# Kernel tuning notes

Hardware: AMD Instinct MI355X
Metric: run time of the kernel (lower is better)

The kernel has to match this reference:

```python
import jax, jax.numpy as jnp
import numpy as np

DIM = 512
N_TOK = 256
BATCH = 512
HIDDEN = int(DIM * 0.2)          # 102
KEEPED = int(256 * 0.5 * 0.4)    # 51 aggregated tokens
NUM_KEEP = int(np.ceil(N_TOK * 0.5))  # 128 kept tokens
EPS_NORM = 1e-12
EPS_LN = 1e-5


def _l2norm(v, axis=-1):
    n = jnp.linalg.norm(v, axis=axis, keepdims=True)
    return v / jnp.maximum(n, EPS_NORM)


def setup_inputs() -> dict:
    key = jax.random.key(0)
    ks = jax.random.split(key, 8)
    x = jax.random.normal(ks[0], (BATCH, N_TOK, DIM), dtype=jnp.float32)
    cross_attention = jax.random.normal(ks[1], (BATCH, N_TOK), dtype=jnp.float32)
    # TokenAggregation params: LayerNorm(dim) -> Linear(dim,hidden) -> GELU -> Linear(hidden,keeped)
    ln_g = jnp.ones((DIM,), jnp.float32)
    ln_b = jnp.zeros((DIM,), jnp.float32)
    s1 = 1.0 / np.sqrt(DIM)
    W1 = jax.random.uniform(ks[2], (DIM, HIDDEN), jnp.float32, -s1, s1)
    b1 = jax.random.uniform(ks[3], (HIDDEN,), jnp.float32, -s1, s1)
    s2 = 1.0 / np.sqrt(HIDDEN)
    W2 = jax.random.uniform(ks[4], (HIDDEN, KEEPED), jnp.float32, -s2, s2)
    b2 = jax.random.uniform(ks[5], (KEEPED,), jnp.float32, -s2, s2)
    scale = jnp.ones((1, 1, 1), jnp.float32)
    return {"x": x, "cross_attention": cross_attention, "ln_g": ln_g, "ln_b": ln_b,
            "W1": W1, "b1": b1, "W2": W2, "b2": b2, "scale": scale}


def reference(x, cross_attention, ln_g, ln_b, W1, b1, W2, b2, scale):
    # ---- scoring: cosine similarity of each token with the mean token ----
    glo = _l2norm(jnp.mean(x, axis=1, keepdims=True))          # [B,1,C]
    self_att = jnp.sum(glo * _l2norm(x), axis=-1)              # [B,N]
    score = self_att + cross_attention                         # [B,N]

    # ---- TokenSparse: sort descending, split keep / non-keep ----
    idx = jnp.argsort(-score, axis=1)                          # [B,N]
    score_sort = jnp.take_along_axis(score, idx, axis=1)       # [B,N] descending
    keep_idx = idx[:, :NUM_KEEP]                               # [B,K]
    non_idx = idx[:, NUM_KEEP:]                                # [B,N-K]
    sel = jnp.take_along_axis(x, keep_idx[:, :, None], axis=1)       # [B,K,C]
    non = jnp.take_along_axis(x, non_idx[:, :, None], axis=1)        # [B,N-K,C]
    non_w = jax.nn.softmax(score_sort[:, NUM_KEEP:], axis=1)[:, :, None]
    extra = jnp.sum(non * non_w, axis=1, keepdims=True)        # [B,1,C]

    # ---- TokenAggregation: LN -> MLP -> softmax weights -> bmm ----
    mu = jnp.mean(sel, axis=-1, keepdims=True)
    var = jnp.mean((sel - mu) ** 2, axis=-1, keepdims=True)
    h = (sel - mu) / jnp.sqrt(var + EPS_LN) * ln_g + ln_b
    h = jax.nn.gelu(h @ W1 + b1, approximate=False)            # [B,K,H]
    w = h @ W2 + b2                                            # [B,K,P]
    w = jnp.swapaxes(w, 1, 2) * scale                          # [B,P,K]
    w = jax.nn.softmax(w, axis=2)
    aggr = jnp.einsum('bpk,bkc->bpc', w, sel)                  # [B,P,C]

    return jnp.concatenate([aggr, extra], axis=1)              # [B,P+1,C]
```

## Files before the change

kernel.cpp:

```cpp
#include <hip/hip_runtime.h>

#define BB 512
#define TT 256
#define DD 512
#define HH 102
#define PP 51
#define NKEEP 128

typedef unsigned short u16;
typedef unsigned int u32;
typedef unsigned long long u64;
typedef float f32x4 __attribute__((ext_vector_type(4)));
typedef short s16x8 __attribute__((ext_vector_type(8)));

#define MFMA16(A, B, C) __builtin_amdgcn_mfma_f32_16x16x32_bf16((A), (B), (C), 0, 0, 0)

#define GLOAD16(gsrc, ldst)                                                     \
  __builtin_amdgcn_global_load_lds(                                             \
      (const __attribute__((address_space(1))) u32*)(gsrc),                     \
      (__attribute__((address_space(3))) u32*)(ldst), 16, 0, 0)

static __device__ __forceinline__ float bf2f(u16 u) {
  u32 v = ((u32)u) << 16;
  float f;
  __builtin_memcpy(&f, &v, 4);
  return f;
}
static __device__ __forceinline__ u16 f2bf(float f) {
  u32 v;
  __builtin_memcpy(&v, &f, 4);
  u32 r = v + 0x7fffu + ((v >> 16) & 1u);
  return (u16)(r >> 16);
}
static __device__ __forceinline__ u32 cvtpk(float a, float b) {
  u32 r;
  asm("v_cvt_pk_bf16_f32 %0, %1, %2" : "=v"(r) : "v"(a), "v"(b));
  return r;
}
static __device__ __forceinline__ float flo16(u32 u) {
  u32 v = u << 16;
  float f;
  __builtin_memcpy(&f, &v, 4);
  return f;
}
static __device__ __forceinline__ float fhi16(u32 u) {
  u32 v = u & 0xffff0000u;
  float f;
  __builtin_memcpy(&f, &v, 4);
  return f;
}
static __device__ __forceinline__ s16x8 mkfrag4(u32 a, u32 b, u32 c, u32 d) {
  u32 t[4] = {a, b, c, d};
  s16x8 f;
  __builtin_memcpy(&f, t, 16);
  return f;
}
static __device__ __forceinline__ s16x8 mkfrag2(u64 a, u64 b) {
  u64 t[2] = {a, b};
  s16x8 f;
  __builtin_memcpy(&f, t, 16);
  return f;
}
static __device__ __forceinline__ u64 trread(u32 addr, int imm) {
  u64 d;
  asm volatile("ds_read_b64_tr_b16 %0, %1 offset:%2" : "=v"(d) : "v"(addr), "i"(imm));
  return d;
}

__global__ __launch_bounds__(1024, 8) void k_score(
    const float* __restrict__ x, const float* __restrict__ ca,
    const float* __restrict__ w1, const float* __restrict__ w2,
    float* __restrict__ out, int* __restrict__ keepg,
    float* __restrict__ muk, float* __restrict__ ivk,
    u16* __restrict__ w1th, u16* __restrict__ w1tl,
    u16* __restrict__ w2th, u16* __restrict__ w2tl) {
  const int tid = threadIdx.x;

  if (blockIdx.x >= BB) {
    const int e0 = (blockIdx.x - BB) * 4096;
#pragma unroll
    for (int i = 0; i < 4; ++i) {
      const int e = e0 + i * 1024 + tid;
      if (e < 57344) {
        const int p = e >> 9, k = e & 511;
        const float v = (p < HH) ? w1[(size_t)k * HH + p] : 0.f;
        const u16 hi = f2bf(v);
        w1th[e] = hi;
        w1tl[e] = f2bf(v - bf2f(hi));
      } else {
        const int e2 = e - 57344;
        const int p = e2 >> 7, j = e2 & 127;
        const float v = (p < PP && j < HH) ? w2[(size_t)j * PP + p] : 0.f;
        const u16 hi = f2bf(v);
        w2th[e2] = hi;
        w2tl[e2] = f2bf(v - bf2f(hi));
      }
    }
    return;
  }

  __shared__ float part[8 * 512];
  __shared__ float glo[DD];
  __shared__ float sc[TT];
  __shared__ float ss[TT];
  __shared__ int perm[TT];
  __shared__ float wq[NKEEP];
  __shared__ float red[128];
  __shared__ float mls[TT], ils[TT];
  int* pc = (int*)part;

  const int b = blockIdx.x;
  const float* xb = x + (size_t)b * TT * DD;

  {
    int c4 = (tid & 127) * 4, tg = tid >> 7;
    float4 a = {0.f, 0.f, 0.f, 0.f};
    const float* p0 = xb + tg * 32 * DD + c4;
    for (int t = 0; t < 32; ++t) {
      float4 v = *(const float4*)(p0 + t * DD);
      a.x += v.x; a.y += v.y; a.z += v.z; a.w += v.w;
    }
    *(float4*)&part[tg * 512 + c4] = a;
  }
  __syncthreads();
  if (tid < 128) {
    int c4 = tid * 4;
    float4 m = {0.f, 0.f, 0.f, 0.f};
    for (int g = 0; g < 8; ++g) {
      float4 v = *(const float4*)&part[g * 512 + c4];
      m.x += v.x; m.y += v.y; m.z += v.z; m.w += v.w;
    }
    m.x *= (1.f / TT); m.y *= (1.f / TT); m.z *= (1.f / TT); m.w *= (1.f / TT);
    *(float4*)&glo[c4] = m;
    red[tid] = m.x * m.x + m.y * m.y + m.z * m.z + m.w * m.w;
  }
  __syncthreads();
  for (int s = 64; s > 0; s >>= 1) {
    if (tid < s) red[tid] += red[tid + s];
    __syncthreads();
  }
  if (tid < 128) {
    float inv = 1.f / fmaxf(sqrtf(red[0]), 1e-12f);
    int c4 = tid * 4;
    float4 m = *(float4*)&glo[c4];
    m.x *= inv; m.y *= inv; m.z *= inv; m.w *= inv;
    *(float4*)&glo[c4] = m;
  }
  __syncthreads();

  {
    const int w = tid >> 6, lane = tid & 63;
    float gl[8];
#pragma unroll
    for (int j = 0; j < 8; ++j) gl[j] = glo[lane * 8 + j];
    for (int i = 0; i < 16; ++i) {
      int t = w * 16 + i;
      const float* xr = xb + t * DD + lane * 8;
      float4 r0 = *(const float4*)xr;
      float4 r1 = *(const float4*)(xr + 4);
      float vs[8] = {r0.x, r0.y, r0.z, r0.w, r1.x, r1.y, r1.z, r1.w};
      float s1 = 0.f, s2 = 0.f, dt = 0.f;
#pragma unroll
      for (int j = 0; j < 8; ++j) {
        s1 += vs[j];
        s2 += vs[j] * vs[j];
        dt += vs[j] * gl[j];
      }
      for (int m = 32; m; m >>= 1) {
        s1 += __shfl_xor(s1, m);
        s2 += __shfl_xor(s2, m);
        dt += __shfl_xor(dt, m);
      }
      if (lane == 0) {
        sc[t] = dt / fmaxf(sqrtf(s2), 1e-12f) + ca[b * TT + t];
        float mu = s1 * (1.f / DD);
        float var = s2 * (1.f / DD) - mu * mu;
        mls[t] = mu;
        ils[t] = rsqrtf(var + 1e-5f);
      }
    }
  }
  __syncthreads();

  {
    int t = tid & 255, ch = tid >> 8;
    float st = sc[t];
    int cnt = 0;
    for (int j = ch * 64; j < ch * 64 + 64; ++j) {
      float sj = sc[j];
      cnt += (sj > st) || (sj == st && j < t);
    }
    pc[ch * 256 + t] = cnt;
  }
  __syncthreads();
  if (tid < 256) {
    int rank = pc[tid] + pc[256 + tid] + pc[512 + tid] + pc[768 + tid];
    perm[rank] = tid;
    ss[rank] = sc[tid];
  }
  __syncthreads();

  if (tid < 128) {
    float e = expf(ss[NKEEP + tid] - ss[NKEEP]);
    wq[tid] = e;
    red[tid] = e;
  }
  __syncthreads();
  for (int s = 64; s > 0; s >>= 1) {
    if (tid < s) red[tid] += red[tid + s];
    __syncthreads();
  }
  if (tid < 128) {
    wq[tid] *= (1.f / red[0]);
    const int pm = perm[tid];
    keepg[b * NKEEP + tid] = pm;
    muk[b * NKEEP + tid] = mls[pm];
    ivk[b * NKEEP + tid] = ils[pm];
  }
  __syncthreads();

  {
    int c4 = (tid & 127) * 4, tg = tid >> 7;
    float4 a = {0.f, 0.f, 0.f, 0.f};
    for (int q = tg * 16; q < tg * 16 + 16; ++q) {
      int tok = perm[NKEEP + q] & 255;
      float w = wq[q];
      float4 v = *(const float4*)(xb + tok * DD + c4);
      a.x += w * v.x; a.y += w * v.y; a.z += w * v.z; a.w += w * v.w;
    }
    *(float4*)&part[tg * 512 + c4] = a;
  }
  __syncthreads();
  if (tid < 128) {
    int c4 = tid * 4;
    float4 m = {0.f, 0.f, 0.f, 0.f};
    for (int g = 0; g < 8; ++g) {
      float4 v = *(const float4*)&part[g * 512 + c4];
      m.x += v.x; m.y += v.y; m.z += v.z; m.w += v.w;
    }
    *(float4*)(out + ((size_t)b * 52 + 51) * DD + c4) = m;
  }
}

__global__ __launch_bounds__(512, 2) void k_fused(
    const float* __restrict__ x,
    const u16* __restrict__ w1th, const u16* __restrict__ w1tl,
    const u16* __restrict__ w2th, const u16* __restrict__ w2tl,
    const float* __restrict__ lng, const float* __restrict__ lnb,
    const float* __restrict__ b1, const float* __restrict__ b2,
    const float* __restrict__ scale, const int* __restrict__ keepg,
    const float* __restrict__ mukg, const float* __restrict__ ivkg,
    float* __restrict__ out) {
  __shared__ __align__(16) char pool[66560];
  __shared__ __align__(16) float lnGs[DD], lnBs[DD];
  __shared__ float mus[NKEEP], ivs[NKEEP];
  __shared__ int keeps[NKEEP];
  __shared__ float b1s[112], b2s[64];
  __shared__ float sscale;

  const int b = blockIdx.x;
  const int tid = threadIdx.x;
  const int w = tid >> 6;
  const int lane = tid & 63;
  const int cl = lane & 15;
  const int g2 = lane >> 4;

  if (tid < NKEEP) {
    keeps[tid] = keepg[b * NKEEP + tid] & 255;
    mus[tid] = mukg[b * NKEEP + tid];
    ivs[tid] = ivkg[b * NKEEP + tid];
  }
  for (int i = tid; i < DD; i += 512) {
    lnGs[i] = lng[i];
    lnBs[i] = lnb[i];
  }
  if (tid < 112) b1s[tid] = (tid < HH) ? b1[tid] : 0.f;
  if (tid < 64) b2s[tid] = (tid < PP) ? b2[tid] : 0.f;
  if (tid == 0) sscale = scale[0];
  __syncthreads();

  const float* xb = x + (size_t)b * TT * DD;

  const int rowm = 16 * w + cl;
  const int tok = keeps[rowm];
  const float mu = mus[rowm], iv = ivs[rowm];
  const float nmuiv = -mu * iv;
  const float* xrow = xb + (size_t)tok * DD;

  const int swz7 = cl & 7;
  const int bA0 = cl * 128 + ((g2 ^ swz7) << 4);
  const int bA1 = cl * 128 + (((4 + g2) ^ swz7) << 4);

  f32x4 acc1[7];
#pragma unroll
  for (int n = 0; n < 7; ++n) acc1[n] = (f32x4){0.f, 0.f, 0.f, 0.f};

#define STAGE_W1(tt, dst)                                                      \
  {                                                                            \
    _Pragma("unroll") for (int i_ = 0; i_ < 4; ++i_) {                         \
      const int j_ = w + 8 * i_;                                               \
      if (j_ < 28) {                                                           \
        const int s_ = j_ * 64 + lane;                                         \
        const int part_ = (j_ >= 14);                                          \
        const int sr_ = s_ - part_ * 896;                                      \
        const int row_ = sr_ >> 3, uu_ = sr_ & 7;                              \
        const u16* src_ = (part_ ? w1tl : w1th) + row_ * 512 + (tt)*64 +       \
                          ((uu_ ^ (row_ & 7)) << 3);                           \
        GLOAD16(src_, (dst) + j_ * 1024);                                      \
      }                                                                        \
    }                                                                          \
  }

  float4 xc0 = *(const float4*)(xrow + g2 * 8);
  float4 xc1 = *(const float4*)(xrow + g2 * 8 + 4);
  float4 xc2 = *(const float4*)(xrow + 32 + g2 * 8);
  float4 xc3 = *(const float4*)(xrow + 32 + g2 * 8 + 4);
  STAGE_W1(0, pool);
  __syncthreads();

#pragma unroll 1
  for (int t = 0; t < 8; ++t) {
    float4 xn0, xn1, xn2, xn3;
    if (t < 7) {
      STAGE_W1(t + 1, pool + ((t + 1) & 1) * 28672);
      const float* xr2 = xrow + (t + 1) * 64 + g2 * 8;
      xn0 = *(const float4*)xr2;
      xn1 = *(const float4*)(xr2 + 4);
      xn2 = *(const float4*)(xr2 + 32);
      xn3 = *(const float4*)(xr2 + 36);
    }
    const char* wbr = pool + (t & 1) * 28672;
#pragma unroll
    for (int kh = 0; kh < 2; ++kh) {
      const int d0 = t * 64 + kh * 32 + g2 * 8;
      const float4 xv0 = kh ? xc2 : xc0;
      const float4 xv1 = kh ? xc3 : xc1;
      const float4 gg0 = *(const float4*)&lnGs[d0];
      const float4 gg1 = *(const float4*)&lnGs[d0 + 4];
      const float4 bb0 = *(const float4*)&lnBs[d0];
      const float4 bb1 = *(const float4*)&lnBs[d0 + 4];
      float y0 = fmaf(fmaf(xv0.x, iv, nmuiv), gg0.x, bb0.x);
      float y1 = fmaf(fmaf(xv0.y, iv, nmuiv), gg0.y, bb0.y);
      float y2 = fmaf(fmaf(xv0.z, iv, nmuiv), gg0.z, bb0.z);
      float y3 = fmaf(fmaf(xv0.w, iv, nmuiv), gg0.w, bb0.w);
      float y4 = fmaf(fmaf(xv1.x, iv, nmuiv), gg1.x, bb1.x);
      float y5 = fmaf(fmaf(xv1.y, iv, nmuiv), gg1.y, bb1.y);
      float y6 = fmaf(fmaf(xv1.z, iv, nmuiv), gg1.z, bb1.z);
      float y7 = fmaf(fmaf(xv1.w, iv, nmuiv), gg1.w, bb1.w);
      u32 h01 = cvtpk(y0, y1), h23 = cvtpk(y2, y3);
      u32 h45 = cvtpk(y4, y5), h67 = cvtpk(y6, y7);
      u32 l01 = cvtpk(y0 - flo16(h01), y1 - fhi16(h01));
      u32 l23 = cvtpk(y2 - flo16(h23), y3 - fhi16(h23));
      u32 l45 = cvtpk(y4 - flo16(h45), y5 - fhi16(h45));
      u32 l67 = cvtpk(y6 - flo16(h67), y7 - fhi16(h67));
      const s16x8 fh = mkfrag4(h01, h23, h45, h67);
      const s16x8 fl = mkfrag4(l01, l23, l45, l67);
      const int bA = kh ? bA1 : bA0;
#pragma unroll
      for (int n = 0; n < 7; ++n) {
        const s16x8 bh = *(const s16x8*)(wbr + n * 2048 + bA);
        const s16x8 bl = *(const s16x8*)(wbr + 14336 + n * 2048 + bA);
        acc1[n] = MFMA16(fh, bh, acc1[n]);
        acc1[n] = MFMA16(fl, bh, acc1[n]);
        acc1[n] = MFMA16(fh, bl, acc1[n]);
      }
    }
    __syncthreads();
    if (t < 7) { xc0 = xn0; xc1 = xn1; xc2 = xn2; xc3 = xn3; }
  }

  char* W2b = pool + 32768;
  {
#pragma unroll
    for (int i = 0; i < 4; ++i) {
      const int j2 = w + 8 * i;
      const int part = (j2 >= 16);
      const int jj = j2 - part * 16;
      const int s = jj * 64 + lane;
      const int row = s >> 4, uu = s & 15;
      const u16* src = (part ? w2tl : w2th) + row * 128 + ((uu ^ (row & 15)) << 3);
      GLOAD16(src, W2b + part * 16384 + jj * 1024);
    }
  }
#pragma unroll
  for (int n = 0; n < 7; ++n) {
    const int col = 16 * n + cl;
    const float bia = b1s[col];
#pragma unroll
    for (int r = 0; r < 4; ++r) {
      const int row = 16 * w + 4 * g2 + r;
      float v = acc1[n][r] + bia;
      float ge = 0.5f * v * (1.f + erff(v * 0.70710678118f));
      const int byteoff = (row * 256 + col * 2) ^ ((row & 7) << 4);
      *(u16*)(pool + byteoff) = f2bf(ge);
    }
  }
  for (int i = tid; i < 1024; i += 512) {
    const int row = i >> 3;
    const int col = 112 + 2 * (i & 7);
    const int byteoff = (row * 256 + col * 2) ^ ((row & 7) << 4);
    *(u32*)(pool + byteoff) = 0u;
  }
  __syncthreads();

  f32x4 acc2[4];
#pragma unroll
  for (int n = 0; n < 4; ++n) acc2[n] = (f32x4){0.f, 0.f, 0.f, 0.f};
  {
    const int row2 = 16 * w + cl;
#pragma unroll
    for (int kk = 0; kk < 4; ++kk) {
      const int byteoff = (row2 * 256 + kk * 64 + g2 * 16) ^ ((row2 & 7) << 4);
      const s16x8 ha = *(const s16x8*)(pool + byteoff);
      const int bB = cl * 256 + (((kk * 4 + g2) ^ cl) << 4);
#pragma unroll
      for (int n = 0; n < 4; ++n) {
        const s16x8 bh = *(const s16x8*)(W2b + n * 4096 + bB);
        const s16x8 bl = *(const s16x8*)(W2b + 16384 + n * 4096 + bB);
        acc2[n] = MFMA16(ha, bh, acc2[n]);
        acc2[n] = MFMA16(ha, bl, acc2[n]);
      }
    }
  }
  __syncthreads();
  float* wt = (float*)(pool + 32768);
  {
    const float scv = sscale;
#pragma unroll
    for (int n = 0; n < 4; ++n) {
      const int p = 16 * n + cl;
#pragma unroll
      for (int r = 0; r < 4; ++r) {
        const int k = 16 * w + 4 * g2 + r;
        wt[p * 132 + k] = (acc2[n][r] + b2s[p]) * scv;
      }
    }
  }
  __syncthreads();

  for (int p = w; p < PP; p += 8) {
    float v0 = wt[p * 132 + lane], v1 = wt[p * 132 + 64 + lane];
    float mx = fmaxf(v0, v1);
    for (int m = 32; m; m >>= 1) mx = fmaxf(mx, __shfl_xor(mx, m));
    float e0 = expf(v0 - mx), e1 = expf(v1 - mx);
    float s = e0 + e1;
    for (int m = 32; m; m >>= 1) s += __shfl_xor(s, m);
    float is = 1.f / s;
    wt[p * 132 + lane] = e0 * is;
    wt[p * 132 + 64 + lane] = e1 * is;
  }
  __syncthreads();

  const int mb = w >> 2;
  const int nsub = w & 3;

  const int c4g = tid & 15;
  const int k0 = tid >> 4;
  const float* xcb = xb + 4 * c4g;
  const int tk0 = keeps[k0], tk1 = keeps[k0 + 32];
  const int tk2 = keeps[k0 + 64], tk3 = keeps[k0 + 96];
  const int base_b = (((c4g >> 2) * 2 + ((k0 >> 2) & 1)) << 9) +
                     ((k0 >> 3) << 7) + ((k0 & 3) << 5) + ((c4g & 3) << 3);

  float4 pv0 = *(const float4*)(xcb + (size_t)tk0 * DD);
  float4 pv1 = *(const float4*)(xcb + (size_t)tk1 * DD);
  float4 pv2 = *(const float4*)(xcb + (size_t)tk2 * DD);
  float4 pv3 = *(const float4*)(xcb + (size_t)tk3 * DD);

  s16x8 ah0[4], al0[4], ah1[4], al1[4];
  {
    const int pr0 = 32 * mb + cl;
    const int pr1 = pr0 + 16;
#pragma unroll
    for (int kk = 0; kk < 4; ++kk) {
      f32x4 wa = *(const f32x4*)&wt[pr0 * 132 + kk * 32 + 8 * g2];
      f32x4 wb = *(const f32x4*)&wt[pr0 * 132 + kk * 32 + 8 * g2 + 4];
      u32 a0 = cvtpk(wa.x, wa.y), a1 = cvtpk(wa.z, wa.w);
      u32 a2 = cvtpk(wb.x, wb.y), a3 = cvtpk(wb.z, wb.w);
      ah0[kk] = mkfrag4(a0, a1, a2, a3);
      al0[kk] = mkfrag4(cvtpk(wa.x - flo16(a0), wa.y - fhi16(a0)),
                        cvtpk(wa.z - flo16(a1), wa.w - fhi16(a1)),
                        cvtpk(wb.x - flo16(a2), wb.y - fhi16(a2)),
                        cvtpk(wb.z - flo16(a3), wb.w - fhi16(a3)));
      f32x4 wc = *(const f32x4*)&wt[pr1 * 132 + kk * 32 + 8 * g2];
      f32x4 wd = *(const f32x4*)&wt[pr1 * 132 + kk * 32 + 8 * g2 + 4];
      u32 c0 = cvtpk(wc.x, wc.y), c1 = cvtpk(wc.z, wc.w);
      u32 c2 = cvtpk(wd.x, wd.y), c3 = cvtpk(wd.z, wd.w);
      ah1[kk] = mkfrag4(c0, c1, c2, c3);
      al1[kk] = mkfrag4(cvtpk(wc.x - flo16(c0), wc.y - fhi16(c0)),
                        cvtpk(wc.z - flo16(c1), wc.w - fhi16(c1)),
                        cvtpk(wd.x - flo16(c2), wd.y - fhi16(c2)),
                        cvtpk(wd.z - flo16(c3), wd.w - fhi16(c3)));
    }
  }
  const u32 trbase = (u32)(size_t)pool + nsub * 1024 + g2 * 128 + 8 * cl;

#define SELW(v, bo)                                                            \
  {                                                                            \
    u32 h01_ = cvtpk((v).x, (v).y), h23_ = cvtpk((v).z, (v).w);                \
    u32 q01_ = cvtpk((v).x - flo16(h01_), (v).y - fhi16(h01_));                \
    u32 q23_ = cvtpk((v).z - flo16(h23_), (v).w - fhi16(h23_));                \
    *(u64*)(pool + (bo)) = ((u64)h23_ << 32) | h01_;                           \
    *(u64*)(pool + 16384 + (bo)) = ((u64)q23_ << 32) | q01_;                   \
  }

#pragma unroll 1
  for (int ch = 0; ch < 8; ++ch) {
    SELW(pv0, base_b);
    SELW(pv1, base_b + 4096);
    SELW(pv2, base_b + 8192);
    SELW(pv3, base_b + 12288);
    __syncthreads();
    float4 nv0, nv1, nv2, nv3;
    if (ch < 7) {
      const float* xnp = xcb + (ch + 1) * 64;
      nv0 = *(const float4*)(xnp + (size_t)tk0 * DD);
      nv1 = *(const float4*)(xnp + (size_t)tk1 * DD);
      nv2 = *(const float4*)(xnp + (size_t)tk2 * DD);
      nv3 = *(const float4*)(xnp + (size_t)tk3 * DD);
    }
    f32x4 acg0 = (f32x4){0.f, 0.f, 0.f, 0.f};
    f32x4 acg1 = (f32x4){0.f, 0.f, 0.f, 0.f};
    u64 th[4][2], tl[4][2];
#pragma unroll
    for (int kk = 0; kk < 4; ++kk) {
      th[kk][0] = trread(trbase, kk * 4096);
      th[kk][1] = trread(trbase, kk * 4096 + 512);
      tl[kk][0] = trread(trbase, kk * 4096 + 16384);
      tl[kk][1] = trread(trbase, kk * 4096 + 16896);
    }
    asm volatile("s_waitcnt lgkmcnt(0)" ::: "memory");
    __builtin_amdgcn_sched_barrier(0);
#pragma unroll
    for (int kk = 0; kk < 4; ++kk) {
      const s16x8 bh = mkfrag2(th[kk][0], th[kk][1]);
      const s16x8 bl = mkfrag2(tl[kk][0], tl[kk][1]);
      acg0 = MFMA16(ah0[kk], bh, acg0);
      acg0 = MFMA16(al0[kk], bh, acg0);
      acg0 = MFMA16(ah0[kk], bl, acg0);
      acg1 = MFMA16(ah1[kk], bh, acg1);
      acg1 = MFMA16(al1[kk], bh, acg1);
      acg1 = MFMA16(ah1[kk], bl, acg1);
    }
    const int ccol = ch * 64 + 16 * nsub + cl;
#pragma unroll
    for (int r = 0; r < 4; ++r) {
      const int p0 = 32 * mb + 4 * g2 + r;
      if (p0 < PP) out[((size_t)b * 52 + p0) * DD + ccol] = acg0[r];
      const int p1 = 32 * mb + 16 + 4 * g2 + r;
      if (p1 < PP) out[((size_t)b * 52 + p1) * DD + ccol] = acg1[r];
    }
    __syncthreads();
    if (ch < 7) { pv0 = nv0; pv1 = nv1; pv2 = nv2; pv3 = nv3; }
  }
}

extern "C" void kernel_launch(void* const* d_in, const int* in_sizes, int n_in,
                              void* d_out, int out_size, void* d_ws, size_t ws_size,
                              hipStream_t stream) {
  const float* x = (const float*)d_in[0];
  const float* ca = (const float*)d_in[1];
  const float* lng = (const float*)d_in[2];
  const float* lnb = (const float*)d_in[3];
  const float* w1 = (const float*)d_in[4];
  const float* b1 = (const float*)d_in[5];
  const float* w2 = (const float*)d_in[6];
  const float* b2 = (const float*)d_in[7];
  const float* scale = (const float*)d_in[8];
  float* out = (float*)d_out;

  char* ws = (char*)d_ws;
  int* keepg = (int*)ws;
  float* muk = (float*)(ws + 262144);
  float* ivk = (float*)(ws + 524288);
  u16* w1th = (u16*)(ws + 786432);
  u16* w1tl = (u16*)(ws + 901120);
  u16* w2th = (u16*)(ws + 1015808);
  u16* w2tl = (u16*)(ws + 1032192);

  k_score<<<BB + 16, 1024, 0, stream>>>(x, ca, w1, w2, out, keepg, muk, ivk,
                                        w1th, w1tl, w2th, w2tl);
  k_fused<<<BB, 512, 0, stream>>>(x, w1th, w1tl, w2th, w2tl, lng, lnb, b1, b2,
                                  scale, keepg, muk, ivk, out);
}
```

Measured before the change: 523.2 us.

## Fuse column-sum and per-token stats into a single pass over x

The scoring kernel used to read each batch's x tile twice: once for the token mean and again for the per-token norm, mean/var and dot with the global mean. It now walks x once in 64-column chunks. Each thread keeps its 16 values in registers while the chunk column sums are reduced through a swizzled LDS buffer, and the dot product is accumulated against those unnormalised sums, with normalisation applied at the end. This halves global reads in this phase at the cost of three barriers per chunk and a larger LDS footprint that may lower occupancy.

```diff
diff --git a/kernel.cpp b/kernel.cpp
--- a/kernel.cpp
+++ b/kernel.cpp
@@ -99,98 +99,119 @@
     return;
   }
 
-  __shared__ float part[8 * 512];
-  __shared__ float glo[DD];
+  __shared__ __align__(16) float xls[256 * 64];
+  __shared__ float part2[1024];
+  __shared__ float cs[64];
+  __shared__ float ctot[512];
   __shared__ float sc[TT];
   __shared__ float ss[TT];
   __shared__ int perm[TT];
   __shared__ float wq[NKEEP];
   __shared__ float red[128];
-  __shared__ float mls[TT], ils[TT];
-  int* pc = (int*)part;
+
+  int* pc = (int*)xls;
+  float* part5 = xls;
+  float* mls = part2;
+  float* ils = part2 + 256;
 
   const int b = blockIdx.x;
   const float* xb = x + (size_t)b * TT * DD;
 
+  const int r = tid >> 2;
+  const int q = tid & 3;
+  const int r7 = r & 7;
+  const int rgA = tid >> 6, jA = tid & 63;
+  const int uA = jA >> 2, sA = jA & 3;
+
+  float s1p = 0.f, s2p = 0.f, dtp = 0.f;
+
+#pragma unroll 1
+  for (int ch = 0; ch < 8; ++ch) {
+    const float* xp = xb + (size_t)r * DD + ch * 64 + q * 16;
+    const float4 v0 = *(const float4*)xp;
+    const float4 v1 = *(const float4*)(xp + 4);
+    const float4 v2 = *(const float4*)(xp + 8);
+    const float4 v3 = *(const float4*)(xp + 12);
+    s1p += (v0.x + v0.y + v0.z + v0.w) + (v1.x + v1.y + v1.z + v1.w) +
+           (v2.x + v2.y + v2.z + v2.w) + (v3.x + v3.y + v3.z + v3.w);
+    s2p += v0.x * v0.x + v0.y * v0.y + v0.z * v0.z + v0.w * v0.w +
+           v1.x * v1.x + v1.y * v1.y + v1.z * v1.z + v1.w * v1.w +
+           v2.x * v2.x + v2.y * v2.y + v2.z * v2.z + v2.w * v2.w +
+           v3.x * v3.x + v3.y * v3.y + v3.z * v3.z + v3.w * v3.w;
+    *(float4*)&xls[r * 64 + (((q * 4 + 0) ^ r7) << 2)] = v0;
+    *(float4*)&xls[r * 64 + (((q * 4 + 1) ^ r7) << 2)] = v1;
+    *(float4*)&xls[r * 64 + (((q * 4 + 2) ^ r7) << 2)] = v2;
+    *(float4*)&xls[r * 64 + (((q * 4 + 3) ^ r7) << 2)] = v3;
+    __syncthreads();
+    {
+      float a = 0.f;
+#pragma unroll
+      for (int rr = 0; rr < 16; ++rr) {
+        a += xls[(rgA * 16 + rr) * 64 + ((uA ^ (rr & 7)) << 2) + sA];
+      }
+      part2[rgA * 64 + jA] = a;
+    }
+    __syncthreads();
+    if (tid < 64) {
+      float c = 0.f;
+#pragma unroll
+      for (int g = 0; g < 16; ++g) c += part2[g * 64 + tid];
+      cs[tid] = c;
+      ctot[ch * 64 + tid] = c;
+    }
+    __syncthreads();
+    {
+      const float4 c0 = *(const float4*)&cs[q * 16];
+      const float4 c1 = *(const float4*)&cs[q * 16 + 4];
+      const float4 c2 = *(const float4*)&cs[q * 16 + 8];
+      const float4 c3 = *(const float4*)&cs[q * 16 + 12];
+      dtp += v0.x * c0.x + v0.y * c0.y + v0.z * c0.z + v0.w * c0.w +
+             v1.x * c1.x + v1.y * c1.y + v1.z * c1.z + v1.w * c1.w +
+             v2.x * c2.x + v2.y * c2.y + v2.z * c2.z + v2.w * c2.w +
+             v3.x * c3.x + v3.y * c3.y + v3.z * c3.z + v3.w * c3.w;
+    }
+  }
+  __syncthreads();
+
+  if (tid < 512) {
+    float cv = ctot[tid];
+    float v = cv * cv;
+    for (int m = 32; m; m >>= 1) v += __shfl_xor(v, m);
+    if ((tid & 63) == 0) red[tid >> 6] = v;
+  }
+  __syncthreads();
+  if (tid == 0) {
+    float cn2 = red[0] + red[1] + red[2] + red[3] + red[4] + red[5] + red[6] + red[7];
+    cs[0] = 1.f / fmaxf(sqrtf(cn2) * (1.f / 256.f), 1e-12f);
+  }
+  __syncthreads();
+
   {
-    int c4 = (tid & 127) * 4, tg = tid >> 7;
-    float4 a = {0.f, 0.f, 0.f, 0.f};
-    const float* p0 = xb + tg * 32 * DD + c4;
-    for (int t = 0; t < 32; ++t) {
-      float4 v = *(const float4*)(p0 + t * DD);
-      a.x += v.x; a.y += v.y; a.z += v.z; a.w += v.w;
-    }
-    *(float4*)&part[tg * 512 + c4] = a;
-  }
-  __syncthreads();
-  if (tid < 128) {
-    int c4 = tid * 4;
-    float4 m = {0.f, 0.f, 0.f, 0.f};
-    for (int g = 0; g < 8; ++g) {
-      float4 v = *(const float4*)&part[g * 512 + c4];
-      m.x += v.x; m.y += v.y; m.z += v.z; m.w += v.w;
-    }
-    m.x *= (1.f / TT); m.y *= (1.f / TT); m.z *= (1.f / TT); m.w *= (1.f / TT);
-    *(float4*)&glo[c4] = m;
-    red[tid] = m.x * m.x + m.y * m.y + m.z * m.z + m.w * m.w;
-  }
-  __syncthreads();
-  for (int s = 64; s > 0; s >>= 1) {
-    if (tid < s) red[tid] += red[tid + s];
-    __syncthreads();
-  }
-  if (tid < 128) {
-    float inv = 1.f / fmaxf(sqrtf(red[0]), 1e-12f);
-    int c4 = tid * 4;
-    float4 m = *(float4*)&glo[c4];
-    m.x *= inv; m.y *= inv; m.z *= inv; m.w *= inv;
-    *(float4*)&glo[c4] = m;
+    float a1 = s1p, a2 = s2p, ad = dtp;
+    a1 += __shfl_xor(a1, 1); a1 += __shfl_xor(a1, 2);
+    a2 += __shfl_xor(a2, 1); a2 += __shfl_xor(a2, 2);
+    ad += __shfl_xor(ad, 1); ad += __shfl_xor(ad, 2);
+    if (q == 0) {
+      const float invc = cs[0];
+      const float self = ad * (1.f / 256.f) * invc;
+      sc[r] = self / fmaxf(sqrtf(a2), 1e-12f) + ca[b * TT + r];
+      const float mu = a1 * (1.f / DD);
+      const float var = a2 * (1.f / DD) - mu * mu;
+      mls[r] = mu;
+      ils[r] = rsqrtf(var + 1e-5f);
+    }
   }
   __syncthreads();
 
   {
-    const int w = tid >> 6, lane = tid & 63;
-    float gl[8];
-#pragma unroll
-    for (int j = 0; j < 8; ++j) gl[j] = glo[lane * 8 + j];
-    for (int i = 0; i < 16; ++i) {
-      int t = w * 16 + i;
-      const float* xr = xb + t * DD + lane * 8;
-      float4 r0 = *(const float4*)xr;
-      float4 r1 = *(const float4*)(xr + 4);
-      float vs[8] = {r0.x, r0.y, r0.z, r0.w, r1.x, r1.y, r1.z, r1.w};
-      float s1 = 0.f, s2 = 0.f, dt = 0.f;
-#pragma unroll
-      for (int j = 0; j < 8; ++j) {
-        s1 += vs[j];
-        s2 += vs[j] * vs[j];
-        dt += vs[j] * gl[j];
-      }
-      for (int m = 32; m; m >>= 1) {
-        s1 += __shfl_xor(s1, m);
-        s2 += __shfl_xor(s2, m);
-        dt += __shfl_xor(dt, m);
-      }
-      if (lane == 0) {
-        sc[t] = dt / fmaxf(sqrtf(s2), 1e-12f) + ca[b * TT + t];
-        float mu = s1 * (1.f / DD);
-        float var = s2 * (1.f / DD) - mu * mu;
-        mls[t] = mu;
-        ils[t] = rsqrtf(var + 1e-5f);
-      }
-    }
-  }
-  __syncthreads();
-
-  {
-    int t = tid & 255, ch = tid >> 8;
+    int t = tid & 255, chh = tid >> 8;
     float st = sc[t];
     int cnt = 0;
-    for (int j = ch * 64; j < ch * 64 + 64; ++j) {
+    for (int j = chh * 64; j < chh * 64 + 64; ++j) {
       float sj = sc[j];
       cnt += (sj > st) || (sj == st && j < t);
     }
-    pc[ch * 256 + t] = cnt;
+    pc[chh * 256 + t] = cnt;
   }
   __syncthreads();
   if (tid < 256) {
@@ -222,20 +243,20 @@
   {
     int c4 = (tid & 127) * 4, tg = tid >> 7;
     float4 a = {0.f, 0.f, 0.f, 0.f};
-    for (int q = tg * 16; q < tg * 16 + 16; ++q) {
-      int tok = perm[NKEEP + q] & 255;
-      float w = wq[q];
+    for (int qq = tg * 16; qq < tg * 16 + 16; ++qq) {
+      int tok = perm[NKEEP + qq] & 255;
+      float w = wq[qq];
       float4 v = *(const float4*)(xb + tok * DD + c4);
       a.x += w * v.x; a.y += w * v.y; a.z += w * v.z; a.w += w * v.w;
     }
-    *(float4*)&part[tg * 512 + c4] = a;
+    *(float4*)&part5[tg * 512 + c4] = a;
   }
   __syncthreads();
   if (tid < 128) {
     int c4 = tid * 4;
     float4 m = {0.f, 0.f, 0.f, 0.f};
     for (int g = 0; g < 8; ++g) {
-      float4 v = *(const float4*)&part[g * 512 + c4];
+      float4 v = *(const float4*)&part5[g * 512 + c4];
       m.x += v.x; m.y += v.y; m.z += v.z; m.w += v.w;
     }
     *(float4*)(out + ((size_t)b * 52 + 51) * DD + c4) = m;
```

Result: faster. 490.0 us (-6.3%).
